# Performance work log

Hardware: AMD Instinct MI355X
Metric: run time of the kernel (lower is better)

## Reference

```python
import jax, jax.numpy as jnp
import numpy as np

N_NODES = 50000
N_EDGES = 1250000
D = 64
EPS = 1e-07


def setup_inputs() -> dict:
    key = jax.random.key(0)
    ks = jax.random.split(key, 10)
    return {
        "node_feats": jax.random.normal(ks[0], (N_NODES, D), jnp.float32),
        "emb0": jax.random.normal(ks[1], (8, D), jnp.float32),
        "emb1": jax.random.normal(ks[2], (4, D), jnp.float32),
        "W": jax.random.normal(ks[3], (D, D), jnp.float32) / np.sqrt(D),
        "b": jnp.zeros((D,), jnp.float32),
        "beta": jnp.ones((1,), jnp.float32),
        "scale": jnp.ones((1,), jnp.float32),
        "src": jax.random.randint(ks[4], (N_EDGES,), 0, N_NODES),
        "dst": jax.random.randint(ks[5], (N_EDGES,), 0, N_NODES),
        "edge_feat0": jax.random.randint(ks[6], (N_EDGES,), 0, 8),
        "edge_feat1": jax.random.randint(ks[7], (N_EDGES,), 0, 4),
    }


def reference(node_feats, emb0, emb1, W, b, beta, scale, src, dst, edge_feat0, edge_feat1):
    n = node_feats.shape[0]
    # edge embeddings summed over categorical feature types
    e = emb0[edge_feat0] + emb1[edge_feat1]              # [E, D]
    # u_add_e then relu + eps
    m = jnp.maximum(node_feats[src] + e, 0.0) + EPS      # [E, D]
    # edge softmax over edges sharing the same destination (per feature dim)
    logits = m * beta                                    # [E, D]
    mx = jax.ops.segment_max(logits, dst, num_segments=n)
    ex = jnp.exp(logits - mx[dst])
    denom = jax.ops.segment_sum(ex, dst, num_segments=n)
    a = ex / denom[dst]                                  # [E, D]
    # scatter-sum aggregation of m * a to destination nodes
    msg = jax.ops.segment_sum(m * a, dst, num_segments=n)  # [N, D]
    # MessageNorm: L2-normalize msg, rescale by ||node_feats|| * scale
    msg_unit = msg / jnp.maximum(
        jnp.linalg.norm(msg, axis=-1, keepdims=True), 1e-12)
    feats_norm = jnp.linalg.norm(node_feats, axis=-1, keepdims=True)
    msg = msg_unit * feats_norm * scale
    # residual + single-layer MLP
    feats = node_feats + msg
    return feats @ W + b
```

## Files before the change

### kernel.cpp

```cpp
#include <hip/hip_runtime.h>

#define NN 50000
#define NE 1250000
#define DD 64
#define KR 391
#define RSH 7
#define RCAP 4096
#define RCSH 12


__global__ __launch_bounds__(512) void k_part(
    const int4* __restrict__ src4, const int4* __restrict__ dst4,
    const int4* __restrict__ ef04, const int4* __restrict__ ef14,
    const float* __restrict__ W, float* __restrict__ Wt,
    int* __restrict__ rcur, unsigned* __restrict__ staging)
{
    __shared__ int hist[KR], rbase[KR], cur[KR];
    const int t  = threadIdx.x;
    const int gb = blockIdx.x;

    for (int i = t; i < KR; i += 512) { hist[i] = 0; cur[i] = 0; }
    if (gb == 0)
        for (int i = t; i < 4096; i += 512)
            Wt[(i & 63) * DD + (i >> 6)] = W[i];
    __syncthreads();

    unsigned pay[8];
    int rr[8];
#pragma unroll
    for (int u = 0; u < 8; ++u) rr[u] = -1;

#pragma unroll
    for (int g = 0; g < 2; ++g) {
        const int i4 = gb * 1024 + t + g * 512;
        if (i4 < NE / 4) {
            const int4 s  = src4[i4], d = dst4[i4];
            const int4 f0 = ef04[i4], f1 = ef14[i4];
            const int ds[4] = {d.x, d.y, d.z, d.w};
            const int ss[4] = {s.x, s.y, s.z, s.w};
            const int a0[4] = {f0.x, f0.y, f0.z, f0.w};
            const int a1[4] = {f1.x, f1.y, f1.z, f1.w};
#pragma unroll
            for (int u = 0; u < 4; ++u) {
                const int k = g * 4 + u;
                rr[k]  = ds[u] >> RSH;
                pay[k] = (unsigned)ss[u] | ((unsigned)(a1[u] * 8 + a0[u]) << 16)
                         | ((unsigned)(ds[u] & 127) << 21);
            }
        }
    }
#pragma unroll
    for (int u = 0; u < 8; ++u)
        if (rr[u] >= 0) atomicAdd(&hist[rr[u]], 1);
    __syncthreads();

    for (int i = t; i < KR; i += 512) {
        const int h = hist[i];
        if (h) rbase[i] = atomicAdd(&rcur[i], h);
    }
    __syncthreads();

#pragma unroll
    for (int u = 0; u < 8; ++u) {
        if (rr[u] >= 0) {
            const int r   = rr[u];
            const int pos = rbase[r] + atomicAdd(&cur[r], 1);
            if (pos < RCAP) staging[(r << RCSH) + pos] = pay[u];
        }
    }
}

__global__ __launch_bounds__(256) void k_bucket(
    const unsigned* __restrict__ staging, const int* __restrict__ rcur,
    int* __restrict__ cnt, unsigned* __restrict__ bucket)
{
    __shared__ unsigned buck[128 * DD];
    __shared__ int ldeg[128];
    const int t = threadIdx.x;
    const int r = blockIdx.x;

    if (t < 128) ldeg[t] = 0;
    __syncthreads();

    const int ne = min(rcur[r], RCAP);
    for (int i = t; i < ne; i += 256) {
        const unsigned p = staging[(r << RCSH) + i];
        const int d = (p >> 21) & 127;
        const int pos = atomicAdd(&ldeg[d], 1);
        if (pos < DD) buck[(d << 6) + pos] = p & 0x1FFFFFu;
    }
    __syncthreads();

    const int base_node = r << RSH;
    const int nnodes = min(128, NN - base_node);
    for (int i = t; i < nnodes * DD; i += 256)
        bucket[((size_t)base_node << 6) + i] = buck[i];
    if (t < nnodes) cnt[base_node + t] = min(ldeg[t], DD);
}

__global__ __launch_bounds__(256, 4) void genconv_agg(
    const float* __restrict__ nf,
    const float* __restrict__ emb0, const float* __restrict__ emb1,
    const float* __restrict__ Wt,  const float* __restrict__ b,
    const float* __restrict__ beta_p, const float* __restrict__ scale_p,
    const int* __restrict__ cnt,
    float* out)
{
    __shared__ __align__(16) float emb_s[32 * DD];
    __shared__ __align__(16) float feat_s[4][DD];

    const int w    = threadIdx.x >> 6;
    const int lane = threadIdx.x & 63;
    const int hl   = lane & 31;
    const int hi   = lane >> 5;

    for (int i = threadIdx.x; i < 32 * DD; i += 256) {
        const int r = i >> 6, c = i & 63;
        emb_s[i] = emb0[(r & 7) * DD + c] + emb1[(r >> 3) * DD + c];
    }

    float4 wc[16];
#pragma unroll
    for (int k = 0; k < 16; ++k)
        wc[k] = *(const float4*)(Wt + lane * DD + 4 * k);

    const float bias  = b[lane];
    const float beta  = beta_p[0];
    const float scale = scale_p[0];
    __syncthreads();

    const float2* __restrict__ nf2  = (const float2*)nf;
    const float2* __restrict__ emb2 = (const float2*)emb_s;
    const unsigned* bucket = (const unsigned*)out;
    const int stride = gridDim.x * 4;

    int node = blockIdx.x * 4 + w;
    unsigned pl = bucket[(size_t)node * DD + lane];
    int cn = min(cnt[node], DD);

    while (node < NN) {
        const int nnext = node + stride;
        unsigned pl_n = 0u;
        int cn_n = 0;
        if (nnext < NN) {
            pl_n = bucket[(size_t)nnext * DD + lane];
            cn_n = cnt[nnext];
        }
        const float2 f2 = nf2[(node << 5) + hl];

        float2 num2 = make_float2(0.f, 0.f);
        float2 den2 = make_float2(0.f, 0.f);

        int j = 0;
        for (; j + 12 <= cn; j += 12) {
            float2 a2[6];
            int eo[6];
#pragma unroll
            for (int u = 0; u < 6; ++u) {
                const unsigned qA =
                    (unsigned)__builtin_amdgcn_readlane((int)pl, j + 2 * u);
                const unsigned qB =
                    (unsigned)__builtin_amdgcn_readlane((int)pl, j + 2 * u + 1);
                const unsigned q = hi ? qB : qA;
                a2[u] = nf2[((q & 0xFFFFu) << 5) + hl];
                eo[u] = (int)(q >> 16) << 5;
            }
#pragma unroll
            for (int u = 0; u < 6; ++u) {
                const float2 e2 = emb2[eo[u] + hl];
                const float mx = fmaxf(a2[u].x + e2.x, 0.f) + 1e-7f;
                const float my = fmaxf(a2[u].y + e2.y, 0.f) + 1e-7f;
                const float xx = __expf(beta * mx);
                const float xy = __expf(beta * my);
                den2.x += xx;               den2.y += xy;
                num2.x = fmaf(mx, xx, num2.x);
                num2.y = fmaf(my, xy, num2.y);
            }
        }
        if (j < cn) {
#pragma unroll
            for (int u = 0; u < 6; ++u) {
                const unsigned qA =
                    (unsigned)__builtin_amdgcn_readlane((int)pl, (j + 2 * u) & 63);
                const unsigned qB =
                    (unsigned)__builtin_amdgcn_readlane((int)pl, (j + 2 * u + 1) & 63);
                const unsigned q = hi ? qB : qA;
                const int row = min((int)(q & 0xFFFFu), NN - 1);
                const float2 a2 = nf2[(row << 5) + hl];
                const float2 e2 = emb2[(((q >> 16) & 31) << 5) + hl];
                const float mx = fmaxf(a2.x + e2.x, 0.f) + 1e-7f;
                const float my = fmaxf(a2.y + e2.y, 0.f) + 1e-7f;
                float xx = __expf(beta * mx);
                float xy = __expf(beta * my);
                const bool valid = (j + 2 * u + hi) < cn;
                xx = valid ? xx : 0.f;
                xy = valid ? xy : 0.f;
                den2.x += xx;               den2.y += xy;
                num2.x = fmaf(mx, xx, num2.x);
                num2.y = fmaf(my, xy, num2.y);
            }
        }

        num2.x += __shfl_xor(num2.x, 32, 64);
        num2.y += __shfl_xor(num2.y, 32, 64);
        den2.x += __shfl_xor(den2.x, 32, 64);
        den2.y += __shfl_xor(den2.y, 32, 64);

        float2 msg2;
        msg2.x = (den2.x > 0.f) ? num2.x / den2.x : 0.f;
        msg2.y = (den2.y > 0.f) ? num2.y / den2.y : 0.f;

        float ss = msg2.x * msg2.x + msg2.y * msg2.y;
        float fs = f2.x * f2.x + f2.y * f2.y;
#pragma unroll
        for (int m = 16; m >= 1; m >>= 1) {
            ss += __shfl_xor(ss, m, 64);
            fs += __shfl_xor(fs, m, 64);
        }

        const float coef =
            (1.0f / fmaxf(sqrtf(ss), 1e-12f)) * sqrtf(fs) * scale;
        float2 feat2;
        feat2.x = f2.x + msg2.x * coef;
        feat2.y = f2.y + msg2.y * coef;

        ((float2*)feat_s[w])[hl] = feat2;

        float acc = bias;
#pragma unroll
        for (int k = 0; k < 16; ++k) {
            const float4 fv = *(const float4*)&feat_s[w][4 * k];
            acc = fmaf(fv.x, wc[k].x, acc);
            acc = fmaf(fv.y, wc[k].y, acc);
            acc = fmaf(fv.z, wc[k].z, acc);
            acc = fmaf(fv.w, wc[k].w, acc);
        }
        out[(size_t)node * DD + lane] = acc;

        node = nnext;
        pl = pl_n;
        cn = min(cn_n, DD);
    }
}

extern "C" void kernel_launch(void* const* d_in, const int* in_sizes, int n_in,
                              void* d_out, int out_size, void* d_ws, size_t ws_size,
                              hipStream_t stream)
{
    const float* nf    = (const float*)d_in[0];
    const float* emb0  = (const float*)d_in[1];
    const float* emb1  = (const float*)d_in[2];
    const float* W     = (const float*)d_in[3];
    const float* b     = (const float*)d_in[4];
    const float* beta  = (const float*)d_in[5];
    const float* scale = (const float*)d_in[6];
    const int* src = (const int*)d_in[7];
    const int* dst = (const int*)d_in[8];
    const int* ef0 = (const int*)d_in[9];
    const int* ef1 = (const int*)d_in[10];

    int*      rcur    = (int*)d_ws;
    int*      cnt     = rcur + 512;
    float*    Wt      = (float*)(cnt + 50048);
    unsigned* staging = (unsigned*)(Wt + 4096);

    hipMemsetAsync(rcur, 0, 512 * sizeof(int), stream);

    k_part<<<(NE / 4 + 1023) / 1024, 512, 0, stream>>>(
        (const int4*)src, (const int4*)dst, (const int4*)ef0, (const int4*)ef1,
        W, Wt, rcur, staging);

    k_bucket<<<KR, 256, 0, stream>>>(staging, rcur, cnt, (unsigned*)d_out);

    genconv_agg<<<4096, 256, 0, stream>>>(
        nf, emb0, emb1, Wt, b, beta, scale, cnt, (float*)d_out);
}
```

Before: 199.9 us.

## Reuse histogram atomics for slots, pad global counters, vectorize edge math, raise occupancy

The partition kernel now keeps the return value of the shared histogram atomic as each edge's local slot, so the second pass of shared atomics on a separate cursor array goes away. The global per-range counters are spaced 16 ints apart, putting each on its own cache line, and the memset grows to cover them. The aggregation kernel's edge math uses 2-wide vector types so the compiler can emit packed float ops. Its launch bounds ask for 6 waves per SIMD instead of 4, which caps register use and may cause spills.

```diff
diff --git a/kernel.cpp b/kernel.cpp
--- a/kernel.cpp
+++ b/kernel.cpp
@@ -8,6 +8,8 @@
 #define RCAP 4096
 #define RCSH 12
 
+typedef float vf2 __attribute__((ext_vector_type(2)));
+
 
 __global__ __launch_bounds__(512) void k_part(
     const int4* __restrict__ src4, const int4* __restrict__ dst4,
@@ -15,24 +17,24 @@
     const float* __restrict__ W, float* __restrict__ Wt,
     int* __restrict__ rcur, unsigned* __restrict__ staging)
 {
-    __shared__ int hist[KR], rbase[KR], cur[KR];
+    __shared__ int hist[KR], rbase[KR];
     const int t  = threadIdx.x;
     const int gb = blockIdx.x;
 
-    for (int i = t; i < KR; i += 512) { hist[i] = 0; cur[i] = 0; }
+    for (int i = t; i < KR; i += 512) hist[i] = 0;
     if (gb == 0)
         for (int i = t; i < 4096; i += 512)
             Wt[(i & 63) * DD + (i >> 6)] = W[i];
     __syncthreads();
 
     unsigned pay[8];
-    int rr[8];
+    int rr[8], lp[8];
 #pragma unroll
     for (int u = 0; u < 8; ++u) rr[u] = -1;
 
 #pragma unroll
     for (int g = 0; g < 2; ++g) {
-        const int i4 = gb * 1024 + t + g * 512;
+        const int i4 = gb * 1024 + g * 512 + t;
         if (i4 < NE / 4) {
             const int4 s  = src4[i4], d = dst4[i4];
             const int4 f0 = ef04[i4], f1 = ef14[i4];
@@ -51,21 +53,20 @@
     }
 #pragma unroll
     for (int u = 0; u < 8; ++u)
-        if (rr[u] >= 0) atomicAdd(&hist[rr[u]], 1);
+        if (rr[u] >= 0) lp[u] = atomicAdd(&hist[rr[u]], 1);
     __syncthreads();
 
     for (int i = t; i < KR; i += 512) {
         const int h = hist[i];
-        if (h) rbase[i] = atomicAdd(&rcur[i], h);
+        if (h) rbase[i] = atomicAdd(&rcur[i << 4], h);
     }
     __syncthreads();
 
 #pragma unroll
     for (int u = 0; u < 8; ++u) {
         if (rr[u] >= 0) {
-            const int r   = rr[u];
-            const int pos = rbase[r] + atomicAdd(&cur[r], 1);
-            if (pos < RCAP) staging[(r << RCSH) + pos] = pay[u];
+            const int pos = rbase[rr[u]] + lp[u];
+            if (pos < RCAP) staging[(rr[u] << RCSH) + pos] = pay[u];
         }
     }
 }
@@ -82,7 +83,7 @@
     if (t < 128) ldeg[t] = 0;
     __syncthreads();
 
-    const int ne = min(rcur[r], RCAP);
+    const int ne = min(rcur[r << 4], RCAP);
     for (int i = t; i < ne; i += 256) {
         const unsigned p = staging[(r << RCSH) + i];
         const int d = (p >> 21) & 127;
@@ -98,7 +99,7 @@
     if (t < nnodes) cnt[base_node + t] = min(ldeg[t], DD);
 }
 
-__global__ __launch_bounds__(256, 4) void genconv_agg(
+__global__ __launch_bounds__(256, 6) void genconv_agg(
     const float* __restrict__ nf,
     const float* __restrict__ emb0, const float* __restrict__ emb1,
     const float* __restrict__ Wt,  const float* __restrict__ b,
@@ -129,10 +130,12 @@
     const float scale = scale_p[0];
     __syncthreads();
 
-    const float2* __restrict__ nf2  = (const float2*)nf;
-    const float2* __restrict__ emb2 = (const float2*)emb_s;
+    const vf2* __restrict__ nf2  = (const vf2*)nf;
+    const vf2* __restrict__ emb2 = (const vf2*)emb_s;
     const unsigned* bucket = (const unsigned*)out;
     const int stride = gridDim.x * 4;
+    const vf2 zero = {0.0f, 0.0f};
+    const vf2 epsv = {1e-7f, 1e-7f};
 
     int node = blockIdx.x * 4 + w;
     unsigned pl = bucket[(size_t)node * DD + lane];
@@ -146,14 +149,13 @@
             pl_n = bucket[(size_t)nnext * DD + lane];
             cn_n = cnt[nnext];
         }
-        const float2 f2 = nf2[(node << 5) + hl];
-
-        float2 num2 = make_float2(0.f, 0.f);
-        float2 den2 = make_float2(0.f, 0.f);
+        const vf2 f2 = nf2[(node << 5) + hl];
+
+        vf2 num2 = zero, den2 = zero;
 
         int j = 0;
         for (; j + 12 <= cn; j += 12) {
-            float2 a2[6];
+            vf2 a2[6];
             int eo[6];
 #pragma unroll
             for (int u = 0; u < 6; ++u) {
@@ -167,14 +169,14 @@
             }
 #pragma unroll
             for (int u = 0; u < 6; ++u) {
-                const float2 e2 = emb2[eo[u] + hl];
-                const float mx = fmaxf(a2[u].x + e2.x, 0.f) + 1e-7f;
-                const float my = fmaxf(a2[u].y + e2.y, 0.f) + 1e-7f;
-                const float xx = __expf(beta * mx);
-                const float xy = __expf(beta * my);
-                den2.x += xx;               den2.y += xy;
-                num2.x = fmaf(mx, xx, num2.x);
-                num2.y = fmaf(my, xy, num2.y);
+                const vf2 e2 = emb2[eo[u] + hl];
+                vf2 m = __builtin_elementwise_max(a2[u] + e2, zero) + epsv;
+                const vf2 bm = m * beta;
+                vf2 x;
+                x.x = __expf(bm.x);
+                x.y = __expf(bm.y);
+                den2 += x;
+                num2 += m * x;
             }
         }
         if (j < cn) {
@@ -186,18 +188,17 @@
                     (unsigned)__builtin_amdgcn_readlane((int)pl, (j + 2 * u + 1) & 63);
                 const unsigned q = hi ? qB : qA;
                 const int row = min((int)(q & 0xFFFFu), NN - 1);
-                const float2 a2 = nf2[(row << 5) + hl];
-                const float2 e2 = emb2[(((q >> 16) & 31) << 5) + hl];
-                const float mx = fmaxf(a2.x + e2.x, 0.f) + 1e-7f;
-                const float my = fmaxf(a2.y + e2.y, 0.f) + 1e-7f;
-                float xx = __expf(beta * mx);
-                float xy = __expf(beta * my);
+                const vf2 a2 = nf2[(row << 5) + hl];
+                const vf2 e2 = emb2[(((q >> 16) & 31) << 5) + hl];
+                vf2 m = __builtin_elementwise_max(a2 + e2, zero) + epsv;
+                const vf2 bm = m * beta;
+                vf2 x;
+                x.x = __expf(bm.x);
+                x.y = __expf(bm.y);
                 const bool valid = (j + 2 * u + hi) < cn;
-                xx = valid ? xx : 0.f;
-                xy = valid ? xy : 0.f;
-                den2.x += xx;               den2.y += xy;
-                num2.x = fmaf(mx, xx, num2.x);
-                num2.y = fmaf(my, xy, num2.y);
+                x = valid ? x : zero;
+                den2 += x;
+                num2 += m * x;
             }
         }
 
@@ -206,7 +207,7 @@
         den2.x += __shfl_xor(den2.x, 32, 64);
         den2.y += __shfl_xor(den2.y, 32, 64);
 
-        float2 msg2;
+        vf2 msg2;
         msg2.x = (den2.x > 0.f) ? num2.x / den2.x : 0.f;
         msg2.y = (den2.y > 0.f) ? num2.y / den2.y : 0.f;
 
@@ -220,11 +221,9 @@
 
         const float coef =
             (1.0f / fmaxf(sqrtf(ss), 1e-12f)) * sqrtf(fs) * scale;
-        float2 feat2;
-        feat2.x = f2.x + msg2.x * coef;
-        feat2.y = f2.y + msg2.y * coef;
-
-        ((float2*)feat_s[w])[hl] = feat2;
+        vf2 feat2 = f2 + msg2 * coef;
+
+        ((vf2*)feat_s[w])[hl] = feat2;
 
         float acc = bias;
 #pragma unroll
@@ -260,11 +259,11 @@
     const int* ef1 = (const int*)d_in[10];
 
     int*      rcur    = (int*)d_ws;
-    int*      cnt     = rcur + 512;
+    int*      cnt     = rcur + KR * 16 + 16;
     float*    Wt      = (float*)(cnt + 50048);
     unsigned* staging = (unsigned*)(Wt + 4096);
 
-    hipMemsetAsync(rcur, 0, 512 * sizeof(int), stream);
+    hipMemsetAsync(rcur, 0, (size_t)(KR * 16 + 16) * sizeof(int), stream);
 
     k_part<<<(NE / 4 + 1023) / 1024, 512, 0, stream>>>(
         (const int4*)src, (const int4*)dst, (const int4*)ef0, (const int4*)ef1,
```

New measurement: 258.6 us. 1.29x slower.
